# Kernel optimization log

Measured on AMD Instinct MI355X. Metric: run time of the kernel, lower is better.

The kernel has to match this reference:

```python
import jax, jax.numpy as jnp
import numpy as np

HEADS = 16
MAX_REL = 128  # max_relative_distance


def setup_inputs() -> dict:
    key = jax.random.key(0)
    ks = jax.random.split(key, 5)
    B, T, L, D = 2, 8, 512, 1024
    return {
        "x": jax.random.normal(ks[0], (B, T, L, D), dtype=jnp.float32),
        "w_qkv": jax.random.normal(ks[1], (D, 3 * D), dtype=jnp.float32) * (D ** -0.5),
        "rel_emb": jax.random.normal(ks[2], (2 * MAX_REL - 1, HEADS), dtype=jnp.float32) * 0.02,
        "w_out": jax.random.normal(ks[3], (D, D), dtype=jnp.float32) * (D ** -0.5),
        "b_out": jax.random.normal(ks[4], (D,), dtype=jnp.float32) * 0.02,
    }


def reference(x, w_qkv, rel_emb, w_out, b_out):
    B, T, L, D = x.shape
    h = HEADS
    dh = D // h
    scale = dh ** -0.5

    xf = x.reshape(B * T, L, D)
    qkv = xf @ w_qkv                                   # (BT, L, 3D)
    q, k, v = jnp.split(qkv, 3, axis=-1)
    q = q.reshape(B * T, L, h, dh)
    k = k.reshape(B * T, L, h, dh)
    v = v.reshape(B * T, L, h, dh)

    attn = jnp.einsum('blhd,bshd->bhls', q, k) * scale  # (BT, h, L, L)

    # relative-position bias: clamp pairwise distances to [-(MAX_REL-1), MAX_REL-1]
    r = jnp.arange(L)
    rel = jnp.clip(r[:, None] - r[None, :], -(MAX_REL - 1), MAX_REL - 1) + (MAX_REL - 1)
    bias = rel_emb[rel]                                 # (L, L, h)
    attn = attn + jnp.transpose(bias, (2, 0, 1))[None]  # broadcast over batch

    attn = jax.nn.softmax(attn, axis=-1)
    out = jnp.einsum('bhls,bshd->blhd', attn, v).reshape(B * T, L, D)
    out = out @ w_out + b_out
    return out.reshape(B, T, L, D)
```

## Files before the change

kernel.cpp:

```cpp
#include <hip/hip_runtime.h>
#include <cstddef>
#include <cstdint>

#define BTN 16
#define LL 512
#define DD 1024
#define NH 16
#define DH 64

using bf8 = __attribute__((ext_vector_type(8))) short;
using fx4 = __attribute__((ext_vector_type(4))) float;

__device__ __forceinline__ unsigned short f2bf(float f) {
  unsigned int u = __float_as_uint(f);
  u += 0x7FFFu + ((u >> 16) & 1u);
  return (unsigned short)(u >> 16);
}

__device__ __forceinline__ fx4 mfma16(bf8 a, bf8 b, fx4 c) {
  return __builtin_amdgcn_mfma_f32_16x16x32_bf16(a, b, c, 0, 0, 0);
}

__device__ __forceinline__ void gld_lds16(const void* g, void* l) {
  __builtin_amdgcn_global_load_lds((const __attribute__((address_space(1))) void*)g,
                                   (__attribute__((address_space(3))) void*)l, 16, 0, 0);
}


__global__ __launch_bounds__(256) void k_cvt(const float* __restrict__ src,
                                             unsigned short* __restrict__ dst) {
  const int i = blockIdx.x * 256 + threadIdx.x;
  const float4 v = ((const float4*)src)[i];
  ushort4 o;
  o.x = f2bf(v.x); o.y = f2bf(v.y); o.z = f2bf(v.z); o.w = f2bf(v.w);
  ((ushort4*)dst)[i] = o;
}

__global__ __launch_bounds__(256) void k_trans(const float* __restrict__ src,
                                               unsigned short* __restrict__ dst,
                                               int R, int C) {
  __shared__ float t[32][33];
  const int tx = threadIdx.x & 31, ty = threadIdx.x >> 5;
  const int c0 = blockIdx.x * 32, r0 = blockIdx.y * 32;
  for (int i = ty; i < 32; i += 8)
    t[i][tx] = src[(size_t)(r0 + i) * C + c0 + tx];
  __syncthreads();
  for (int i = ty; i < 32; i += 8)
    dst[(size_t)(c0 + i) * R + r0 + tx] = f2bf(t[tx][i]);
}


__device__ __forceinline__ void gemm_core(const unsigned short* __restrict__ A,
                                          const unsigned short* __restrict__ B,
                                          unsigned short* Al, unsigned short* Bl,
                                          int m0, int n0, fx4 (&acc)[4][4]) {
  const int tid = threadIdx.x;
  const int lane = tid & 63, wave = tid >> 6;
  const int quad = lane >> 4, l16 = lane & 15;
  const int wr = (wave >> 1) * 64, wc = (wave & 1) * 64;
  const int rl = lane >> 3;
  const int sg = (lane & 7) ^ rl;
  const unsigned short* pa = A + (size_t)(m0 + wave * 32 + rl) * 1024 + sg * 8;
  const unsigned short* pb = B + (size_t)(n0 + wave * 32 + rl) * 1024 + sg * 8;
  unsigned short* la = Al + wave * 2048;
  unsigned short* lb = Bl + wave * 2048;

  for (int kt = 0; kt < 1024; kt += 64) {
    __syncthreads();
#pragma unroll
    for (int i = 0; i < 4; ++i) {
      gld_lds16(pa + kt + i * 8 * 1024, la + i * 512);
      gld_lds16(pb + kt + i * 8 * 1024, lb + i * 512);
    }
    __syncthreads();
#pragma unroll
    for (int kk = 0; kk < 2; ++kk) {
      bf8 av[4], bv[4];
#pragma unroll
      for (int mi = 0; mi < 4; ++mi) {
        const int row = wr + mi * 16 + l16;
        av[mi] = *(const bf8*)(Al + row * 64 + (((kk * 4 + quad) ^ (l16 & 7)) * 8));
      }
#pragma unroll
      for (int nj = 0; nj < 4; ++nj) {
        const int row = wc + nj * 16 + l16;
        bv[nj] = *(const bf8*)(Bl + row * 64 + (((kk * 4 + quad) ^ (l16 & 7)) * 8));
      }
#pragma unroll
      for (int mi = 0; mi < 4; ++mi)
#pragma unroll
        for (int nj = 0; nj < 4; ++nj)
          acc[mi][nj] = mfma16(av[mi], bv[nj], acc[mi][nj]);
    }
  }
}

__global__ __launch_bounds__(256, 4) void k_gemm_qkv(const unsigned short* __restrict__ xbf,
                                                     const unsigned short* __restrict__ wT,
                                                     unsigned short* __restrict__ qws,
                                                     unsigned short* __restrict__ kws,
                                                     unsigned short* __restrict__ vws) {
  __shared__ unsigned short Al[128 * 64];
  __shared__ unsigned short Bl[128 * 64];
  const int m0 = blockIdx.y * 128, n0 = blockIdx.x * 128;
  fx4 acc[4][4];
  const fx4 zero = {0.f, 0.f, 0.f, 0.f};
#pragma unroll
  for (int mi = 0; mi < 4; ++mi)
#pragma unroll
    for (int nj = 0; nj < 4; ++nj) acc[mi][nj] = zero;

  gemm_core(xbf, wT, Al, Bl, m0, n0, acc);

  const int lane = threadIdx.x & 63, wave = threadIdx.x >> 6;
  const int quad = lane >> 4, l16 = lane & 15;
  const int wr = (wave >> 1) * 64, wc = (wave & 1) * 64;
  const int which = n0 >> 10;
#pragma unroll
  for (int mi = 0; mi < 4; ++mi)
#pragma unroll
    for (int nj = 0; nj < 4; ++nj) {
      const int gn = n0 + wc + nj * 16 + l16;
      const int rem = gn & 1023;
      const int hh = rem >> 6, dd = rem & 63;
#pragma unroll
      for (int rr = 0; rr < 4; ++rr) {
        const int gm = m0 + wr + mi * 16 + quad * 4 + rr;
        const int bth = gm >> 9, ll = gm & 511;
        const unsigned short v = f2bf(acc[mi][nj][rr]);
        const size_t bhh = (size_t)(bth * NH + hh);
        if (which == 0)      qws[(bhh * LL + ll) * DH + dd] = v;
        else if (which == 1) kws[(bhh * LL + ll) * DH + dd] = v;
        else                 vws[(bhh * DH + dd) * LL + ll] = v;
      }
    }
}

__global__ __launch_bounds__(256, 4) void k_gemm_out(const unsigned short* __restrict__ obf,
                                                     const unsigned short* __restrict__ wT,
                                                     const float* __restrict__ bout,
                                                     float* __restrict__ out) {
  __shared__ unsigned short Al[128 * 64];
  __shared__ unsigned short Bl[128 * 64];
  const int m0 = blockIdx.y * 128, n0 = blockIdx.x * 128;
  fx4 acc[4][4];
  const fx4 zero = {0.f, 0.f, 0.f, 0.f};
#pragma unroll
  for (int mi = 0; mi < 4; ++mi)
#pragma unroll
    for (int nj = 0; nj < 4; ++nj) acc[mi][nj] = zero;

  gemm_core(obf, wT, Al, Bl, m0, n0, acc);

  const int lane = threadIdx.x & 63, wave = threadIdx.x >> 6;
  const int quad = lane >> 4, l16 = lane & 15;
  const int wr = (wave >> 1) * 64, wc = (wave & 1) * 64;
#pragma unroll
  for (int nj = 0; nj < 4; ++nj) {
    const int gn = n0 + wc + nj * 16 + l16;
    const float bb = bout[gn];
#pragma unroll
    for (int mi = 0; mi < 4; ++mi)
#pragma unroll
      for (int rr = 0; rr < 4; ++rr) {
        const int gm = m0 + wr + mi * 16 + quad * 4 + rr;
        out[(size_t)gm * 1024 + gn] = acc[mi][nj][rr] + bb;
      }
  }
}


#define LDP 136

__global__ __launch_bounds__(256, 2) void k_attn(const unsigned short* __restrict__ qw,
                                                 const unsigned short* __restrict__ kw,
                                                 const unsigned short* __restrict__ vw,
                                                 const float* __restrict__ rel,
                                                 unsigned short* __restrict__ ow) {
  __shared__ unsigned short Kl[128 * 64];
  __shared__ unsigned short Vl[64 * 128];
  __shared__ unsigned short Pl[128 * LDP];
  __shared__ float rell[255];

  const int tid = threadIdx.x;
  const int wave = tid >> 6, lane = tid & 63;
  const int quad = lane >> 4, l16 = lane & 15;
  const int bh = blockIdx.x >> 2, qt = blockIdx.x & 3;
  const int bth = bh >> 4, h = bh & 15;

  if (tid < 255) rell[tid] = rel[tid * NH + h];

  bf8 qf[2][2];
  const size_t qbase = (size_t)bh * (LL * DH) + (size_t)(qt * 128 + wave * 32) * DH;
#pragma unroll
  for (int mi = 0; mi < 2; ++mi)
#pragma unroll
    for (int kk = 0; kk < 2; ++kk)
      qf[mi][kk] = *(const bf8*)(qw + qbase + (mi * 16 + l16) * DH + kk * 32 + quad * 8);

  fx4 O[2][4];
  fx4 lS[2];
  const fx4 zero = {0.f, 0.f, 0.f, 0.f};
#pragma unroll
  for (int mi = 0; mi < 2; ++mi) {
    lS[mi] = zero;
#pragma unroll
    for (int no = 0; no < 4; ++no) O[mi][no] = zero;
  }

  const int rk = lane >> 3, sgk = (lane & 7) ^ rk;
  const int rv = lane >> 4;
  const unsigned short* kbase = kw + (size_t)bh * (LL * DH) + (size_t)(wave * 32 + rk) * 64 + sgk * 8;
  const unsigned short* vbase = vw + (size_t)bh * (DH * LL);
  unsigned short* kdst = Kl + wave * 2048;
  unsigned short* vdst = Vl + wave * 2048;

#pragma unroll
  for (int i = 0; i < 4; ++i)
    gld_lds16(kbase + (size_t)(i * 8) * 64, kdst + i * 512);

  for (int st = 0; st < 4; ++st) {
    __syncthreads();
#pragma unroll
    for (int i = 0; i < 4; ++i) {
      const int rowv = wave * 16 + i * 4 + rv;
      const int sgv = (lane & 15) ^ (rowv & 15);
      gld_lds16(vbase + (size_t)rowv * 512 + st * 128 + sgv * 8, vdst + i * 512);
    }
    __syncthreads();

    fx4 S[2][8];
#pragma unroll
    for (int mi = 0; mi < 2; ++mi)
#pragma unroll
      for (int nj = 0; nj < 8; ++nj) S[mi][nj] = zero;
#pragma unroll
    for (int kk = 0; kk < 2; ++kk) {
      bf8 bk[8];
#pragma unroll
      for (int nj = 0; nj < 8; ++nj) {
        const int row = nj * 16 + l16;
        bk[nj] = *(const bf8*)(Kl + row * 64 + (((kk * 4 + quad) ^ (l16 & 7)) * 8));
      }
#pragma unroll
      for (int mi = 0; mi < 2; ++mi)
#pragma unroll
        for (int nj = 0; nj < 8; ++nj)
          S[mi][nj] = mfma16(qf[mi][kk], bk[nj], S[mi][nj]);
    }

    const int delta = qt - st;
    if (delta >= 2 || delta <= -2) {
      const float cb = (delta >= 2) ? rell[254] : rell[0];
#pragma unroll
      for (int mi = 0; mi < 2; ++mi)
#pragma unroll
        for (int nj = 0; nj < 8; ++nj)
#pragma unroll
          for (int rr = 0; rr < 4; ++rr)
            S[mi][nj][rr] = __expf(fmaf(S[mi][nj][rr], 0.125f, cb));
    } else if (delta == 0) {
#pragma unroll
      for (int mi = 0; mi < 2; ++mi)
#pragma unroll
        for (int rr = 0; rr < 4; ++rr) {
          const int base = wave * 32 + mi * 16 + quad * 4 + rr - l16 + 127;
#pragma unroll
          for (int nj = 0; nj < 8; ++nj)
            S[mi][nj][rr] = __expf(fmaf(S[mi][nj][rr], 0.125f, rell[base - nj * 16]));
        }
    } else {
#pragma unroll
      for (int mi = 0; mi < 2; ++mi)
#pragma unroll
        for (int rr = 0; rr < 4; ++rr) {
          const int base = delta * 128 + wave * 32 + mi * 16 + quad * 4 + rr - l16 + 127;
#pragma unroll
          for (int nj = 0; nj < 8; ++nj) {
            int idx = base - nj * 16;
            idx = idx < 0 ? 0 : (idx > 254 ? 254 : idx);
            S[mi][nj][rr] = __expf(fmaf(S[mi][nj][rr], 0.125f, rell[idx]));
          }
        }
    }

#pragma unroll
    for (int mi = 0; mi < 2; ++mi)
#pragma unroll
      for (int nj = 0; nj < 8; ++nj)
#pragma unroll
        for (int rr = 0; rr < 4; ++rr)
          Pl[(wave * 32 + mi * 16 + quad * 4 + rr) * LDP + nj * 16 + l16] = f2bf(S[mi][nj][rr]);
    __syncthreads();

    if (st < 3) {
#pragma unroll
      for (int i = 0; i < 4; ++i)
        gld_lds16(kbase + (size_t)((st + 1) * 128 + i * 8) * 64, kdst + i * 512);
    }

    const bf8 ones = {0x3F80, 0x3F80, 0x3F80, 0x3F80, 0x3F80, 0x3F80, 0x3F80, 0x3F80};
#pragma unroll
    for (int kk = 0; kk < 4; ++kk) {
      bf8 ap[2], bv[4];
#pragma unroll
      for (int mi = 0; mi < 2; ++mi)
        ap[mi] = *(const bf8*)(Pl + (wave * 32 + mi * 16 + l16) * LDP + kk * 32 + quad * 8);
#pragma unroll
      for (int no = 0; no < 4; ++no) {
        const int row = no * 16 + l16;
        bv[no] = *(const bf8*)(Vl + row * 128 + (((kk * 4 + quad) ^ l16) * 8));
      }
#pragma unroll
      for (int mi = 0; mi < 2; ++mi) {
#pragma unroll
        for (int no = 0; no < 4; ++no)
          O[mi][no] = mfma16(ap[mi], bv[no], O[mi][no]);
        lS[mi] = mfma16(ap[mi], ones, lS[mi]);
      }
    }
  }

#pragma unroll
  for (int mi = 0; mi < 2; ++mi)
#pragma unroll
    for (int rr = 0; rr < 4; ++rr) {
      const float inv = __builtin_amdgcn_rcpf(lS[mi][rr]);
      const int gm = bth * LL + qt * 128 + wave * 32 + mi * 16 + quad * 4 + rr;
#pragma unroll
      for (int no = 0; no < 4; ++no) {
        const int gn = h * DH + no * 16 + l16;
        ow[(size_t)gm * DD + gn] = f2bf(O[mi][no][rr] * inv);
      }
    }
}


extern "C" void kernel_launch(void* const* d_in, const int* in_sizes, int n_in,
                              void* d_out, int out_size, void* d_ws, size_t ws_size,
                              hipStream_t stream) {
  const float* x    = (const float*)d_in[0];
  const float* wqkv = (const float*)d_in[1];
  const float* rel  = (const float*)d_in[2];
  const float* wout = (const float*)d_in[3];
  const float* bout = (const float*)d_in[4];
  float* out = (float*)d_out;

  char* ws = (char*)d_ws;
  unsigned short* xbf   = (unsigned short*)(ws);
  unsigned short* wqkvT = (unsigned short*)(ws + 16777216);
  unsigned short* woutT = (unsigned short*)(ws + 23068672);
  unsigned short* qws   = (unsigned short*)(ws + 25165824);
  unsigned short* kws   = (unsigned short*)(ws + 41943040);
  unsigned short* vws   = (unsigned short*)(ws + 58720256);
  unsigned short* ows   = (unsigned short*)(ws + 75497472);

  k_cvt<<<dim3(8192), dim3(256), 0, stream>>>(x, xbf);
  k_trans<<<dim3(96, 32), dim3(256), 0, stream>>>(wqkv, wqkvT, 1024, 3072);
  k_trans<<<dim3(32, 32), dim3(256), 0, stream>>>(wout, woutT, 1024, 1024);
  k_gemm_qkv<<<dim3(24, 64), dim3(256), 0, stream>>>(xbf, wqkvT, qws, kws, vws);
  k_attn<<<dim3(1024), dim3(256), 0, stream>>>(qws, kws, vws, rel, ows);
  k_gemm_out<<<dim3(8, 64), dim3(256), 0, stream>>>(ows, woutT, bout, out);
}
```

Before: 250.3 us.

## Double-buffer LDS tiles in the GEMM core to overlap loads with MFMA

The shared GEMM core for the QKV and output projections now alternates between two LDS buffers. The global-to-LDS copy of the next K tile is issued before the MFMA work on the current tile, and the K loop is unrolled by two. The goal is to hide global load latency behind matrix math and cut the barrier stalls between load and compute. In exchange, LDS use per block doubles and the occupancy hint in launch bounds drops from 4 to 2, which may limit latency hiding across blocks.

```diff
diff --git a/kernel.cpp b/kernel.cpp
--- a/kernel.cpp
+++ b/kernel.cpp
@@ -50,9 +50,43 @@
 }
 
 
+__device__ __forceinline__ void gemm_stage(const unsigned short* pa, const unsigned short* pb,
+                                           unsigned short* la, unsigned short* lb, int kt) {
+#pragma unroll
+  for (int i = 0; i < 4; ++i) {
+    gld_lds16(pa + kt + i * 8 * 1024, la + i * 512);
+    gld_lds16(pb + kt + i * 8 * 1024, lb + i * 512);
+  }
+}
+
+__device__ __forceinline__ void gemm_compute(const unsigned short* Al, const unsigned short* Bl,
+                                             int wr, int wc, int quad, int l16,
+                                             fx4 (&acc)[4][4]) {
+#pragma unroll
+  for (int kk = 0; kk < 2; ++kk) {
+    bf8 av[4], bv[4];
+#pragma unroll
+    for (int mi = 0; mi < 4; ++mi) {
+      const int row = wr + mi * 16 + l16;
+      av[mi] = *(const bf8*)(Al + row * 64 + (((kk * 4 + quad) ^ (l16 & 7)) * 8));
+    }
+#pragma unroll
+    for (int nj = 0; nj < 4; ++nj) {
+      const int row = wc + nj * 16 + l16;
+      bv[nj] = *(const bf8*)(Bl + row * 64 + (((kk * 4 + quad) ^ (l16 & 7)) * 8));
+    }
+#pragma unroll
+    for (int mi = 0; mi < 4; ++mi)
+#pragma unroll
+      for (int nj = 0; nj < 4; ++nj)
+        acc[mi][nj] = mfma16(av[mi], bv[nj], acc[mi][nj]);
+  }
+}
+
 __device__ __forceinline__ void gemm_core(const unsigned short* __restrict__ A,
                                           const unsigned short* __restrict__ B,
-                                          unsigned short* Al, unsigned short* Bl,
+                                          unsigned short* Al0, unsigned short* Bl0,
+                                          unsigned short* Al1, unsigned short* Bl1,
                                           int m0, int n0, fx4 (&acc)[4][4]) {
   const int tid = threadIdx.x;
   const int lane = tid & 63, wave = tid >> 6;
@@ -62,46 +96,30 @@
   const int sg = (lane & 7) ^ rl;
   const unsigned short* pa = A + (size_t)(m0 + wave * 32 + rl) * 1024 + sg * 8;
   const unsigned short* pb = B + (size_t)(n0 + wave * 32 + rl) * 1024 + sg * 8;
-  unsigned short* la = Al + wave * 2048;
-  unsigned short* lb = Bl + wave * 2048;
-
-  for (int kt = 0; kt < 1024; kt += 64) {
-    __syncthreads();
-#pragma unroll
-    for (int i = 0; i < 4; ++i) {
-      gld_lds16(pa + kt + i * 8 * 1024, la + i * 512);
-      gld_lds16(pb + kt + i * 8 * 1024, lb + i * 512);
-    }
-    __syncthreads();
-#pragma unroll
-    for (int kk = 0; kk < 2; ++kk) {
-      bf8 av[4], bv[4];
-#pragma unroll
-      for (int mi = 0; mi < 4; ++mi) {
-        const int row = wr + mi * 16 + l16;
-        av[mi] = *(const bf8*)(Al + row * 64 + (((kk * 4 + quad) ^ (l16 & 7)) * 8));
-      }
-#pragma unroll
-      for (int nj = 0; nj < 4; ++nj) {
-        const int row = wc + nj * 16 + l16;
-        bv[nj] = *(const bf8*)(Bl + row * 64 + (((kk * 4 + quad) ^ (l16 & 7)) * 8));
-      }
-#pragma unroll
-      for (int mi = 0; mi < 4; ++mi)
-#pragma unroll
-        for (int nj = 0; nj < 4; ++nj)
-          acc[mi][nj] = mfma16(av[mi], bv[nj], acc[mi][nj]);
-    }
-  }
-}
-
-__global__ __launch_bounds__(256, 4) void k_gemm_qkv(const unsigned short* __restrict__ xbf,
+  unsigned short* la0 = Al0 + wave * 2048;
+  unsigned short* lb0 = Bl0 + wave * 2048;
+  unsigned short* la1 = Al1 + wave * 2048;
+  unsigned short* lb1 = Bl1 + wave * 2048;
+
+  gemm_stage(pa, pb, la0, lb0, 0);
+#pragma unroll
+  for (int kt = 0; kt < 1024; kt += 128) {
+    __syncthreads();
+    if (kt + 64 < 1024) gemm_stage(pa, pb, la1, lb1, kt + 64);
+    gemm_compute(Al0, Bl0, wr, wc, quad, l16, acc);
+    __syncthreads();
+    if (kt + 128 < 1024) gemm_stage(pa, pb, la0, lb0, kt + 128);
+    gemm_compute(Al1, Bl1, wr, wc, quad, l16, acc);
+  }
+}
+
+__global__ __launch_bounds__(256, 2) void k_gemm_qkv(const unsigned short* __restrict__ xbf,
                                                      const unsigned short* __restrict__ wT,
                                                      unsigned short* __restrict__ qws,
                                                      unsigned short* __restrict__ kws,
                                                      unsigned short* __restrict__ vws) {
-  __shared__ unsigned short Al[128 * 64];
-  __shared__ unsigned short Bl[128 * 64];
+  __shared__ unsigned short Al[2][128 * 64];
+  __shared__ unsigned short Bl[2][128 * 64];
   const int m0 = blockIdx.y * 128, n0 = blockIdx.x * 128;
   fx4 acc[4][4];
   const fx4 zero = {0.f, 0.f, 0.f, 0.f};
@@ -110,7 +128,7 @@
 #pragma unroll
     for (int nj = 0; nj < 4; ++nj) acc[mi][nj] = zero;
 
-  gemm_core(xbf, wT, Al, Bl, m0, n0, acc);
+  gemm_core(xbf, wT, Al[0], Bl[0], Al[1], Bl[1], m0, n0, acc);
 
   const int lane = threadIdx.x & 63, wave = threadIdx.x >> 6;
   const int quad = lane >> 4, l16 = lane & 15;
@@ -136,12 +154,12 @@
     }
 }
 
-__global__ __launch_bounds__(256, 4) void k_gemm_out(const unsigned short* __restrict__ obf,
+__global__ __launch_bounds__(256, 2) void k_gemm_out(const unsigned short* __restrict__ obf,
                                                      const unsigned short* __restrict__ wT,
                                                      const float* __restrict__ bout,
                                                      float* __restrict__ out) {
-  __shared__ unsigned short Al[128 * 64];
-  __shared__ unsigned short Bl[128 * 64];
+  __shared__ unsigned short Al[2][128 * 64];
+  __shared__ unsigned short Bl[2][128 * 64];
   const int m0 = blockIdx.y * 128, n0 = blockIdx.x * 128;
   fx4 acc[4][4];
   const fx4 zero = {0.f, 0.f, 0.f, 0.f};
@@ -150,7 +168,7 @@
 #pragma unroll
     for (int nj = 0; nj < 4; ++nj) acc[mi][nj] = zero;
 
-  gemm_core(obf, wT, Al, Bl, m0, n0, acc);
+  gemm_core(obf, wT, Al[0], Bl[0], Al[1], Bl[1], m0, n0, acc);
 
   const int lane = threadIdx.x & 63, wave = threadIdx.x >> 6;
   const int quad = lane >> 4, l16 = lane & 15;
```

Measured after the change: 255.5 us. 2.1% more time.
